# Performance work log

Hardware: AMD Instinct MI355X
Metric: run time of the kernel (lower is better)

## Reference

```python
import jax, jax.numpy as jnp
import numpy as np

B, Wd, C, H, F = 48, 88, 256, 32, 1024
NH_SELF, NH_CROSS = 8, 8


def _ln(x, g, b, eps=1e-5):
    mu = x.mean(-1, keepdims=True)
    var = ((x - mu) ** 2).mean(-1, keepdims=True)
    return (x - mu) / jnp.sqrt(var + eps) * g + b


def setup_inputs() -> dict:
    key = jax.random.key(0)
    ks = jax.random.split(key, 16)
    s = 0.02  # weight init scale
    d = {
        'pooled_features': jax.random.normal(ks[0], (B, Wd, C), jnp.float32),
        'features': jax.random.normal(ks[1], (B, C, H, Wd), jnp.float32),
        'self_pe': jax.random.normal(ks[2], (Wd, C), jnp.float32),
        'cross_pe': jax.random.normal(ks[3], (H, C), jnp.float32),
    }
    # LayerNorm params
    for n in ['ln_qs', 'ln_vs', 'ln_qc', 'ln_kv', 'ln_vc', 'ln_ffn']:
        d[n + '_g'] = jnp.ones((C,), jnp.float32)
        d[n + '_b'] = jnp.zeros((C,), jnp.float32)
    # attention projections (stored [in,out]; y = x @ W + b)
    names = ['Wq_s', 'Wk_s', 'Wv_s', 'Wp_s', 'Wq_c', 'Wk_c', 'Wv_c', 'Wp_c']
    for i, n in enumerate(names):
        d[n] = jax.random.normal(ks[4 + i], (C, C), jnp.float32) * s
    for n in ['bq_s', 'bv_s', 'bp_s', 'bq_c', 'bv_c', 'bp_c']:
        d[n] = jnp.zeros((C,), jnp.float32)
    # FFN
    d['W1'] = jax.random.normal(ks[12], (C, F), jnp.float32) * s
    d['b1'] = jnp.zeros((F,), jnp.float32)
    d['W2'] = jax.random.normal(ks[13], (F, C), jnp.float32) * s
    d['b2'] = jnp.zeros((C,), jnp.float32)
    return d


def reference(pooled_features, features, self_pe, cross_pe,
              ln_qs_g, ln_qs_b, ln_vs_g, ln_vs_b,
              ln_qc_g, ln_qc_b, ln_kv_g, ln_kv_b, ln_vc_g, ln_vc_b,
              ln_ffn_g, ln_ffn_b,
              Wq_s, bq_s, Wk_s, Wv_s, bv_s, Wp_s, bp_s,
              Wq_c, bq_c, Wk_c, Wv_c, bv_c, Wp_c, bp_c,
              W1, b1, W2, b2):
    b, w, c = pooled_features.shape
    h = features.shape[2]
    ds = c // NH_SELF
    dc = c // NH_CROSS

    # ---- cross attention first (op_order='cross_first', with_pe=True) ----
    xq = pooled_features                                  # [B,W,C]
    qn = _ln(xq, ln_qc_g, ln_qc_b)
    kv = jnp.transpose(features, (0, 3, 2, 1))            # [B,W,H,C]
    kn = _ln(kv + cross_pe[None, None], ln_kv_g, ln_kv_b)
    vn = _ln(kv, ln_vc_g, ln_vc_b)
    q = (qn @ Wq_c + bq_c).reshape(b, w, NH_CROSS, dc)    # query len 1 per column
    k = (kn @ Wk_c).reshape(b, w, h, NH_CROSS, dc)
    v = (vn @ Wv_c + bv_c).reshape(b, w, h, NH_CROSS, dc)
    attn = jnp.einsum('bwhd,bwkhd->bwhk', q, k) * (dc ** -0.5)
    attn = jax.nn.softmax(attn, axis=-1)
    out = jnp.einsum('bwhk,bwkhd->bwhd', attn, v).reshape(b, w, c)
    x = out @ Wp_c + bp_c + xq

    # ---- self attention over width tokens ----
    qn = _ln(x + self_pe[None], ln_qs_g, ln_qs_b)
    vn = _ln(x, ln_vs_g, ln_vs_b)
    q = (qn @ Wq_s + bq_s).reshape(b, w, NH_SELF, ds)
    k = (qn @ Wk_s).reshape(b, w, NH_SELF, ds)
    v = (vn @ Wv_s + bv_s).reshape(b, w, NH_SELF, ds)
    attn = jnp.einsum('bnhd,bmhd->bhnm', q, k) * (ds ** -0.5)
    attn = jax.nn.softmax(attn, axis=-1)
    out = jnp.einsum('bhnm,bmhd->bnhd', attn, v).reshape(b, w, c)
    x = out @ Wp_s + bp_s + x

    # ---- FFN (mmcv FFN, num_fcs=2, GELU, identity residual) ----
    hdn = _ln(x, ln_ffn_g, ln_ffn_b)
    hdn = jax.nn.gelu(hdn @ W1 + b1, approximate=False) @ W2 + b2
    return x + hdn
```

## Files before the change

kernel.cpp:

```cpp
#include <hip/hip_runtime.h>
#include <math.h>

#define B_   48
#define W_   88
#define C_   256
#define H_   32
#define F_   1024
#define BW_  (B_ * W_)
#define BWH_ (B_ * W_ * H_)
#define HW_  (H_ * W_)

typedef float  f32x4  __attribute__((ext_vector_type(4)));
typedef __bf16 bf16x8 __attribute__((ext_vector_type(8)));

__device__ __forceinline__ unsigned short f2bf(float f) {
  union { float f; unsigned int u; } v; v.f = f;
  unsigned int r = v.u + 0x7FFFu + ((v.u >> 16) & 1u);
  return (unsigned short)(r >> 16);
}
__device__ __forceinline__ float bf2f(unsigned short h) {
  union { unsigned int u; float f; } v; v.u = ((unsigned int)h) << 16;
  return v.f;
}
__device__ __forceinline__ unsigned int pack2(float a, float b) {
  return (unsigned int)f2bf(a) | ((unsigned int)f2bf(b) << 16);
}

__global__ __launch_bounds__(256) void prep_all(
    const float* __restrict__ Wq_s, const float* __restrict__ Wk_s,
    const float* __restrict__ Wv_s, const float* __restrict__ Wp_s,
    const float* __restrict__ W1, const float* __restrict__ W2,
    const float* __restrict__ Wq_c, const float* __restrict__ Wk_c,
    const float* __restrict__ Wv_c, const float* __restrict__ Wp_c,
    const float* __restrict__ bq_s, const float* __restrict__ bv_s,
    const float* __restrict__ bq_c, const float* __restrict__ bv_c,
    const float* __restrict__ bp_c,
    const float* __restrict__ pooled,
    const float* __restrict__ ln_qc_g, const float* __restrict__ ln_qc_b,
    const float* __restrict__ cross_pe,
    unsigned short* __restrict__ wqkvs, unsigned short* __restrict__ wps,
    unsigned short* __restrict__ w1t, unsigned short* __restrict__ w2t,
    unsigned short* __restrict__ mqk, unsigned short* __restrict__ mvp,
    float* __restrict__ bqk, float* __restrict__ bvp,
    float* __restrict__ bqkvs, unsigned short* __restrict__ qn_c,
    float* __restrict__ pes) {
  __shared__ float smem[256 * 33 + 4 * 33];
  int blk = blockIdx.x, t = threadIdx.x;

  if (blk < 768) {
    const float* src; unsigned short* dst; int Cc, R, tile;
    if (blk < 64)       { src = Wq_s; dst = wqkvs;          Cc = 256;  R = 256;  tile = blk; }
    else if (blk < 128) { src = Wk_s; dst = wqkvs + 65536;  Cc = 256;  R = 256;  tile = blk - 64; }
    else if (blk < 192) { src = Wv_s; dst = wqkvs + 131072; Cc = 256;  R = 256;  tile = blk - 128; }
    else if (blk < 256) { src = Wp_s; dst = wps;            Cc = 256;  R = 256;  tile = blk - 192; }
    else if (blk < 512) { src = W1;   dst = w1t;            Cc = 1024; R = 256;  tile = blk - 256; }
    else                { src = W2;   dst = w2t;            Cc = 256;  R = 1024; tile = blk - 512; }
    int tcn = Cc >> 5;
    int tr = tile / tcn, tc = tile % tcn;
    float (*lds)[33] = (float(*)[33])smem;
    int r = t >> 3, c4 = (t & 7) * 4;
    float4 v = *(const float4*)(src + (size_t)(tr * 32 + r) * Cc + tc * 32 + c4);
    lds[r][c4 + 0] = v.x; lds[r][c4 + 1] = v.y; lds[r][c4 + 2] = v.z; lds[r][c4 + 3] = v.w;
    __syncthreads();
    int rd = t >> 3, cd4 = (t & 7) * 4;
    unsigned int u0 = pack2(lds[cd4 + 0][rd], lds[cd4 + 1][rd]);
    unsigned int u1 = pack2(lds[cd4 + 2][rd], lds[cd4 + 3][rd]);
    uint2 u; u.x = u0; u.y = u1;
    *(uint2*)(dst + (size_t)(tc * 32 + rd) * R + tr * 32 + cd4) = u;
  } else if (blk < 1280) {
    int lb = blk - 768;
    int h = lb >> 6, cb = lb & 63;
    float (*wq)[33] = (float(*)[33])smem;
    float (*wk)[33] = (float(*)[33])(smem + 256 * 33);
#pragma unroll
    for (int p = 0; p < 8; p++) {
      int dp = (t >> 3) + 32 * p, d4 = (t & 7) * 4;
      float4 v = *(const float4*)(Wq_c + (size_t)dp * 256 + 32 * h + d4);
      wq[dp][d4 + 0] = v.x; wq[dp][d4 + 1] = v.y; wq[dp][d4 + 2] = v.z; wq[dp][d4 + 3] = v.w;
    }
    if (t < 128) {
      int c_l = t >> 5, dd = t & 31;
      wk[c_l][dd] = Wk_c[(size_t)(cb * 4 + c_l) * 256 + 32 * h + dd];
    }
    __syncthreads();
    const float scale = 0.17677669529663689f;
    int c_l = t >> 6, ln = t & 63;
    int n = 256 * h + cb * 4 + c_l;
#pragma unroll
    for (int j = 0; j < 4; j++) {
      int dp = ln + 64 * j;
      float acc = 0.f;
#pragma unroll
      for (int dd = 0; dd < 32; dd++) acc += wq[dp][dd] * wk[c_l][dd];
      mqk[(size_t)n * 256 + dp] = f2bf(acc * scale);
    }
    if (ln == 0) {
      float bb = 0.f;
#pragma unroll
      for (int dd = 0; dd < 32; dd++) bb += bq_c[32 * h + dd] * wk[c_l][dd];
      bqk[n] = bb * scale;
    }
  } else if (blk < 1792) {
    int lb = blk - 1280;
    int h = lb >> 6, db = lb & 63;
    float (*wv)[33] = (float(*)[33])smem;
    float (*wp)[33] = (float(*)[33])(smem + 256 * 33);
#pragma unroll
    for (int p = 0; p < 8; p++) {
      int c = (t >> 3) + 32 * p, d4 = (t & 7) * 4;
      float4 v = *(const float4*)(Wv_c + (size_t)c * 256 + 32 * h + d4);
      wv[c][d4 + 0] = v.x; wv[c][d4 + 1] = v.y; wv[c][d4 + 2] = v.z; wv[c][d4 + 3] = v.w;
    }
    if (t < 128) {
      int d_l = t >> 5, dd = t & 31;
      wp[d_l][dd] = Wp_c[(size_t)(32 * h + dd) * 256 + db * 4 + d_l];
    }
    __syncthreads();
    int d_l = t >> 6, ln = t & 63;
    int d = db * 4 + d_l;
#pragma unroll
    for (int j = 0; j < 4; j++) {
      int c = ln + 64 * j;
      float acc = 0.f;
#pragma unroll
      for (int dd = 0; dd < 32; dd++) acc += wv[c][dd] * wp[d_l][dd];
      mvp[(size_t)d * 2048 + 256 * h + c] = f2bf(acc);
    }
  } else if (blk == 1792) {
    float acc = bp_c[t];
    for (int dp = 0; dp < 256; dp++) acc += bv_c[dp] * Wp_c[(size_t)dp * 256 + t];
    bvp[t] = acc;
    bqkvs[t] = bq_s[t]; bqkvs[256 + t] = 0.f; bqkvs[512 + t] = bv_s[t];
  } else if (blk < 6017) {
    int row = blk - 1793, c = t;
    float v = pooled[(size_t)row * C_ + c];
    float s1 = v, s2 = v * v;
#pragma unroll
    for (int m = 32; m > 0; m >>= 1) {
      s1 += __shfl_xor(s1, m, 64); s2 += __shfl_xor(s2, m, 64);
    }
    float* red = smem;
    int wave = c >> 6;
    if ((c & 63) == 0) { red[wave] = s1; red[4 + wave] = s2; }
    __syncthreads();
    s1 = red[0] + red[1] + red[2] + red[3];
    s2 = red[4] + red[5] + red[6] + red[7];
    float mu = s1 * (1.f / C_);
    float rs = rsqrtf(s2 * (1.f / C_) - mu * mu + 1e-5f);
    qn_c[(size_t)row * C_ + c] = f2bf((v - mu) * rs * ln_qc_g[c] + ln_qc_b[c]);
  } else {
    int h = t >> 3, seg = t & 7;
    const float* pr = cross_pe + (size_t)h * 256 + seg * 32;
    float s1 = 0.f, s2 = 0.f;
#pragma unroll
    for (int i = 0; i < 32; i++) { float v = pr[i]; s1 += v; s2 += v * v; }
    s1 += __shfl_xor(s1, 1, 8); s2 += __shfl_xor(s2, 1, 8);
    s1 += __shfl_xor(s1, 2, 8); s2 += __shfl_xor(s2, 2, 8);
    s1 += __shfl_xor(s1, 4, 8); s2 += __shfl_xor(s2, 4, 8);
    if (seg == 0) { pes[2 * h] = s1; pes[2 * h + 1] = s2; }
  }
}

__global__ __launch_bounds__(128, 2) void cross_fused(
    const float* __restrict__ features, const float* __restrict__ cross_pe,
    const unsigned short* __restrict__ qt_g,
    const float* __restrict__ g_kv, const float* __restrict__ b_kv,
    const float* __restrict__ g_vc, const float* __restrict__ b_vc,
    const float* __restrict__ pes,
    unsigned short* __restrict__ ctx_g) {
  __shared__ __attribute__((aligned(16))) float stage[2 * 4 * 268];
  const int p = blockIdx.x;
  const int xcd = p & 7, slot = p >> 3;
  const int b = xcd + 8 * (slot / 22);
  const int w0 = (slot % 22) * 4;
  const int t = threadIdx.x;
  const int bw0 = b * 88 + w0;
  const int w = t >> 5, c8 = t & 31, cbase = c8 << 3;

  float qg[8][8], Qg[8], Qb[8];
  {
    float gk8[8], bk8[8];
    float4 u0 = *(const float4*)(g_kv + cbase), u1 = *(const float4*)(g_kv + cbase + 4);
    gk8[0]=u0.x; gk8[1]=u0.y; gk8[2]=u0.z; gk8[3]=u0.w;
    gk8[4]=u1.x; gk8[5]=u1.y; gk8[6]=u1.z; gk8[7]=u1.w;
    u0 = *(const float4*)(b_kv + cbase); u1 = *(const float4*)(b_kv + cbase + 4);
    bk8[0]=u0.x; bk8[1]=u0.y; bk8[2]=u0.z; bk8[3]=u0.w;
    bk8[4]=u1.x; bk8[5]=u1.y; bk8[6]=u1.z; bk8[7]=u1.w;
    const unsigned short* qrow = qt_g + (size_t)(bw0 + w) * 2048 + cbase;
#pragma unroll
    for (int hd = 0; hd < 8; hd++) {
      bf16x8 qv = *(const bf16x8*)(qrow + hd * 256);
      float sg = 0.f, sb = 0.f;
#pragma unroll
      for (int i = 0; i < 8; i++) {
        float qf = (float)qv[i];
        qg[hd][i] = qf * gk8[i];
        sg += qg[hd][i];
        sb += qf * bk8[i];
      }
      Qg[hd] = sg; Qb[hd] = sb;
    }
#pragma unroll
    for (int m = 1; m < 32; m <<= 1) {
#pragma unroll
      for (int hd = 0; hd < 8; hd++) {
        Qg[hd] += __shfl_xor(Qg[hd], m, 32);
        Qb[hd] += __shfl_xor(Qb[hd], m, 32);
      }
    }
  }

  float accA[8][8];
  float accB[8], l[8];
#pragma unroll
  for (int hd = 0; hd < 8; hd++) {
    accB[hd] = 0.f; l[hd] = 0.f;
#pragma unroll
    for (int i = 0; i < 8; i++) accA[hd][i] = 0.f;
  }

  const float* fbase = features + (size_t)b * (C_ * HW_) + w0;
  float4 x0 = *(const float4*)(fbase + (size_t)t * HW_);
  float4 x1 = *(const float4*)(fbase + (size_t)(t + 128) * HW_);
  float4 y0 = *(const float4*)(fbase + (size_t)t * HW_ + 88);
  float4 y1 = *(const float4*)(fbase + (size_t)(t + 128) * HW_ + 88);

#pragma unroll 2
  for (int h = 0; h < 32; ++h) {
    float* st = stage + (h & 1) * (4 * 268);
    st[0 * 268 + t] = x0.x; st[1 * 268 + t] = x0.y;
    st[2 * 268 + t] = x0.z; st[3 * 268 + t] = x0.w;
    st[0 * 268 + 128 + t] = x1.x; st[1 * 268 + 128 + t] = x1.y;
    st[2 * 268 + 128 + t] = x1.z; st[3 * 268 + 128 + t] = x1.w;
    asm volatile("s_waitcnt lgkmcnt(0)" ::: "memory");
    __builtin_amdgcn_s_barrier();
    asm volatile("" ::: "memory");
    if (h < 30) {
      x0 = *(const float4*)(fbase + (size_t)t * HW_ + (h + 2) * 88);
      x1 = *(const float4*)(fbase + (size_t)(t + 128) * HW_ + (h + 2) * 88);
    }
    const float* sr = st + w * 268 + cbase;
    float4 v0 = *(const float4*)(sr);
    float4 v1 = *(const float4*)(sr + 4);
    float vls[8] = {v0.x, v0.y, v0.z, v0.w, v1.x, v1.y, v1.z, v1.w};
    float4 q0 = *(const float4*)(cross_pe + h * 256 + cbase);
    float4 q1 = *(const float4*)(cross_pe + h * 256 + cbase + 4);
    float pe8[8] = {q0.x, q0.y, q0.z, q0.w, q1.x, q1.y, q1.z, q1.w};
    float s1 = 0.f, s2 = 0.f, sp = 0.f;
    float vp[8];
#pragma unroll
    for (int i = 0; i < 8; i++) {
      float v = vls[i];
      vp[i] = v + pe8[i];
      s1 += v; s2 += v * v; sp += v * pe8[i];
    }
    float S[8];
#pragma unroll
    for (int hd = 0; hd < 8; hd++) {
      float a = 0.f;
#pragma unroll
      for (int i = 0; i < 8; i++) a += qg[hd][i] * vp[i];
      S[hd] = a;
    }
#pragma unroll
    for (int m = 1; m < 32; m <<= 1) {
      s1 += __shfl_xor(s1, m, 32);
      s2 += __shfl_xor(s2, m, 32);
      sp += __shfl_xor(sp, m, 32);
#pragma unroll
      for (int hd = 0; hd < 8; hd++) S[hd] += __shfl_xor(S[hd], m, 32);
    }
    float mu_v = s1 * (1.f / 256.f);
    float rs_v = rsqrtf(s2 * (1.f / 256.f) - mu_v * mu_v + 1e-5f);
    float mu_k = (s1 + pes[2 * h]) * (1.f / 256.f);
    float rs_k = rsqrtf((s2 + 2.f * sp + pes[2 * h + 1]) * (1.f / 256.f)
                        - mu_k * mu_k + 1e-5f);
#pragma unroll
    for (int hd = 0; hd < 8; hd++) {
      float sc = rs_k * (S[hd] - mu_k * Qg[hd]) + Qb[hd];
      float e = __expf(sc);
      float er = e * rs_v;
      l[hd] += e;
      accB[hd] += er * mu_v;
#pragma unroll
      for (int i = 0; i < 8; i++) accA[hd][i] += er * vls[i];
    }
    float4 t0 = x0, t1 = x1;
    x0 = y0; x1 = y1;
    y0 = t0; y1 = t1;
  }
  float gv8[8], bv8[8];
  {
    float4 u0 = *(const float4*)(g_vc + cbase), u1 = *(const float4*)(g_vc + cbase + 4);
    gv8[0]=u0.x; gv8[1]=u0.y; gv8[2]=u0.z; gv8[3]=u0.w;
    gv8[4]=u1.x; gv8[5]=u1.y; gv8[6]=u1.z; gv8[7]=u1.w;
    u0 = *(const float4*)(b_vc + cbase); u1 = *(const float4*)(b_vc + cbase + 4);
    bv8[0]=u0.x; bv8[1]=u0.y; bv8[2]=u0.z; bv8[3]=u0.w;
    bv8[4]=u1.x; bv8[5]=u1.y; bv8[6]=u1.z; bv8[7]=u1.w;
  }
  unsigned short* orow = ctx_g + (size_t)(bw0 + w) * 2048 + cbase;
#pragma unroll
  for (int hd = 0; hd < 8; hd++) {
    float inv = 1.f / l[hd];
    unsigned short pk[8];
#pragma unroll
    for (int i = 0; i < 8; i++)
      pk[i] = f2bf(gv8[i] * (accA[hd][i] - accB[hd]) * inv + bv8[i]);
    *(uint4*)(orow + hd * 256) = *(uint4*)pk;
  }
}

__global__ __launch_bounds__(256) void ln_rows(
    const float* __restrict__ x,
    const float* __restrict__ g, const float* __restrict__ bta,
    unsigned short* __restrict__ out) {
  int row = blockIdx.x, c = threadIdx.x;
  float v = x[(size_t)row * C_ + c];
  float s1 = v, s2 = v * v;
#pragma unroll
  for (int m = 32; m > 0; m >>= 1) {
    s1 += __shfl_xor(s1, m, 64);
    s2 += __shfl_xor(s2, m, 64);
  }
  __shared__ float red[8];
  int wave = c >> 6;
  if ((c & 63) == 0) { red[wave] = s1; red[4 + wave] = s2; }
  __syncthreads();
  s1 = red[0] + red[1] + red[2] + red[3];
  s2 = red[4] + red[5] + red[6] + red[7];
  float mu = s1 * (1.f / C_);
  float rs = rsqrtf(s2 * (1.f / C_) - mu * mu + 1e-5f);
  out[(size_t)row * C_ + c] = f2bf((v - mu) * rs * g[c] + bta[c]);
}

__global__ __launch_bounds__(256) void ln_dual(
    const float* __restrict__ x, const float* __restrict__ pe,
    const float* __restrict__ g1, const float* __restrict__ b1a,
    const float* __restrict__ g2, const float* __restrict__ b2a,
    unsigned short* __restrict__ out1, unsigned short* __restrict__ out2) {
  int row = blockIdx.x, c = threadIdx.x;
  float v = x[(size_t)row * C_ + c];
  float vp = v + pe[(size_t)(row % 88) * C_ + c];
  float s1 = v, s2 = v * v, t1 = vp, t2 = vp * vp;
#pragma unroll
  for (int m = 32; m > 0; m >>= 1) {
    s1 += __shfl_xor(s1, m, 64); s2 += __shfl_xor(s2, m, 64);
    t1 += __shfl_xor(t1, m, 64); t2 += __shfl_xor(t2, m, 64);
  }
  __shared__ float red[16];
  int wave = c >> 6;
  if ((c & 63) == 0) {
    red[wave] = s1; red[4 + wave] = s2; red[8 + wave] = t1; red[12 + wave] = t2;
  }
  __syncthreads();
  s1 = red[0] + red[1] + red[2] + red[3];
  s2 = red[4] + red[5] + red[6] + red[7];
  t1 = red[8] + red[9] + red[10] + red[11];
  t2 = red[12] + red[13] + red[14] + red[15];
  float mu = s1 * (1.f / C_), rs = rsqrtf(s2 * (1.f / C_) - mu * mu + 1e-5f);
  float mup = t1 * (1.f / C_), rsp = rsqrtf(t2 * (1.f / C_) - mup * mup + 1e-5f);
  out1[(size_t)row * C_ + c] = f2bf((vp - mup) * rsp * g1[c] + b1a[c]);
  out2[(size_t)row * C_ + c] = f2bf((v - mu) * rs * g2[c] + b2a[c]);
}

__global__ __launch_bounds__(256) void gemm_bt(
    const unsigned short* __restrict__ A, const unsigned short* __restrict__ Bt,
    int M, int N, int K,
    const float* __restrict__ bias, const float* __restrict__ resid,
    float* __restrict__ outF, unsigned short* __restrict__ outB, int act_gelu) {
  __shared__ __attribute__((aligned(16))) unsigned short As[64][32];
  __shared__ __attribute__((aligned(16))) unsigned short Bs[64][32];
  const int tiles_n = N >> 6;
  const int bm = blockIdx.x / tiles_n;
  const int bn = blockIdx.x % tiles_n;
  const int tid = threadIdx.x;
  const int wave = tid >> 6, lane = tid & 63;
  const int quad = lane >> 4, lr = lane & 15;
  const int wm = (wave >> 1) << 5, wn = (wave & 1) << 5;
  const int lrow = tid >> 2;
  const int lcol = (tid & 3) << 3;
  const size_t a_base = (size_t)(bm * 64 + lrow) * K + lcol;
  const size_t b_base = (size_t)(bn * 64 + lrow) * K + lcol;
  f32x4 acc[2][2] = {};
  uint4 areg = *(const uint4*)(A + a_base);
  uint4 breg = *(const uint4*)(Bt + b_base);
  for (int k0 = 0; k0 < K; k0 += 32) {
    *(uint4*)&As[lrow][lcol] = areg;
    *(uint4*)&Bs[lrow][lcol] = breg;
    __syncthreads();
    if (k0 + 32 < K) {
      areg = *(const uint4*)(A + a_base + k0 + 32);
      breg = *(const uint4*)(Bt + b_base + k0 + 32);
    }
    bf16x8 af0 = *(const bf16x8*)&As[wm + lr][quad << 3];
    bf16x8 af1 = *(const bf16x8*)&As[wm + 16 + lr][quad << 3];
    bf16x8 bf0 = *(const bf16x8*)&Bs[wn + lr][quad << 3];
    bf16x8 bf1 = *(const bf16x8*)&Bs[wn + 16 + lr][quad << 3];
    acc[0][0] = __builtin_amdgcn_mfma_f32_16x16x32_bf16(af0, bf0, acc[0][0], 0, 0, 0);
    acc[0][1] = __builtin_amdgcn_mfma_f32_16x16x32_bf16(af0, bf1, acc[0][1], 0, 0, 0);
    acc[1][0] = __builtin_amdgcn_mfma_f32_16x16x32_bf16(af1, bf0, acc[1][0], 0, 0, 0);
    acc[1][1] = __builtin_amdgcn_mfma_f32_16x16x32_bf16(af1, bf1, acc[1][1], 0, 0, 0);
    __syncthreads();
  }
#pragma unroll
  for (int i = 0; i < 2; i++)
#pragma unroll
    for (int j = 0; j < 2; j++)
#pragma unroll
      for (int rr = 0; rr < 4; rr++) {
        int row = bm * 64 + wm + i * 16 + quad * 4 + rr;
        int col = bn * 64 + wn + j * 16 + lr;
        float val = acc[i][j][rr];
        if (bias) val += bias[col];
        if (act_gelu) val = 0.5f * val * (1.f + erff(val * 0.70710678118654752f));
        if (resid) val += resid[(size_t)row * N + col];
        if (outF) outF[(size_t)row * N + col] = val;
        else outB[(size_t)row * N + col] = f2bf(val);
      }
}

__global__ __launch_bounds__(256) void gemm_bt_st(
    const unsigned short* __restrict__ A, const unsigned short* __restrict__ Bt,
    int M, int N, int K, int ldc,
    const float* __restrict__ bias, float* __restrict__ outF) {
  __shared__ __attribute__((aligned(16))) unsigned short As[64][32];
  __shared__ __attribute__((aligned(16))) unsigned short Bs[64][32];
  const int tiles_n = N >> 6;
  const int bm = blockIdx.x / tiles_n;
  const int bn = blockIdx.x % tiles_n;
  const int tid = threadIdx.x;
  const int wave = tid >> 6, lane = tid & 63;
  const int quad = lane >> 4, lr = lane & 15;
  const int wm = (wave >> 1) << 5, wn = (wave & 1) << 5;
  const int lrow = tid >> 2;
  const int lcol = (tid & 3) << 3;
  const size_t a_base = (size_t)(bm * 64 + lrow) * K + lcol;
  const size_t b_base = (size_t)(bn * 64 + lrow) * K + lcol;
  f32x4 acc[2][2] = {};
  uint4 areg = *(const uint4*)(A + a_base);
  uint4 breg = *(const uint4*)(Bt + b_base);
  for (int k0 = 0; k0 < K; k0 += 32) {
    *(uint4*)&As[lrow][lcol] = areg;
    *(uint4*)&Bs[lrow][lcol] = breg;
    __syncthreads();
    if (k0 + 32 < K) {
      areg = *(const uint4*)(A + a_base + k0 + 32);
      breg = *(const uint4*)(Bt + b_base + k0 + 32);
    }
    bf16x8 af0 = *(const bf16x8*)&As[wm + lr][quad << 3];
    bf16x8 af1 = *(const bf16x8*)&As[wm + 16 + lr][quad << 3];
    bf16x8 bf0 = *(const bf16x8*)&Bs[wn + lr][quad << 3];
    bf16x8 bf1 = *(const bf16x8*)&Bs[wn + 16 + lr][quad << 3];
    acc[0][0] = __builtin_amdgcn_mfma_f32_16x16x32_bf16(af0, bf0, acc[0][0], 0, 0, 0);
    acc[0][1] = __builtin_amdgcn_mfma_f32_16x16x32_bf16(af0, bf1, acc[0][1], 0, 0, 0);
    acc[1][0] = __builtin_amdgcn_mfma_f32_16x16x32_bf16(af1, bf0, acc[1][0], 0, 0, 0);
    acc[1][1] = __builtin_amdgcn_mfma_f32_16x16x32_bf16(af1, bf1, acc[1][1], 0, 0, 0);
    __syncthreads();
  }
#pragma unroll
  for (int i = 0; i < 2; i++)
#pragma unroll
    for (int j = 0; j < 2; j++)
#pragma unroll
      for (int rr = 0; rr < 4; rr++) {
        int row = bm * 64 + wm + i * 16 + quad * 4 + rr;
        int col = bn * 64 + wn + j * 16 + lr;
        outF[(size_t)row * ldc + col] = acc[i][j][rr] + bias[col];
      }
}

__global__ __launch_bounds__(192) void self_attn3(
    const float* __restrict__ qkv, unsigned short* __restrict__ out) {
  int b = blockIdx.x >> 3;
  int h = blockIdx.x & 7;
  int t = threadIdx.x;
  __shared__ float kl[88][33];
  __shared__ float vl[88][33];
  for (int i = t; i < 704; i += 192) {
    int m = i >> 3, d4 = (i & 7) << 2;
    float4 kv4 = *(const float4*)(qkv + (size_t)(b * 88 + m) * 768 + 256 + h * 32 + d4);
    float4 vv4 = *(const float4*)(qkv + (size_t)(b * 88 + m) * 768 + 512 + h * 32 + d4);
    kl[m][d4 + 0] = kv4.x; kl[m][d4 + 1] = kv4.y; kl[m][d4 + 2] = kv4.z; kl[m][d4 + 3] = kv4.w;
    vl[m][d4 + 0] = vv4.x; vl[m][d4 + 1] = vv4.y; vl[m][d4 + 2] = vv4.z; vl[m][d4 + 3] = vv4.w;
  }
  __syncthreads();
  int r = t >> 1, dh = t & 1;
  if (r < 88) {
    const float* qrow = qkv + (size_t)(b * 88 + r) * 768 + h * 32;
    float qr[32];
#pragma unroll
    for (int g = 0; g < 8; g++) {
      float4 q4 = *(const float4*)(qrow + g * 4);
      qr[g * 4 + 0] = q4.x; qr[g * 4 + 1] = q4.y; qr[g * 4 + 2] = q4.z; qr[g * 4 + 3] = q4.w;
    }
    float sreg[44];
    float mx = -1e30f;
    int m0 = dh * 44;
    for (int mi = 0; mi < 44; mi++) {
      const float* krow = kl[m0 + mi];
      float s = 0.f;
#pragma unroll
      for (int d = 0; d < 32; d++) s += qr[d] * krow[d];
      s *= 0.17677669529663689f;
      sreg[mi] = s;
      mx = fmaxf(mx, s);
    }
    mx = fmaxf(mx, __shfl_xor(mx, 1, 64));
    float sum = 0.f;
    for (int mi = 0; mi < 44; mi++) { float e = __expf(sreg[mi] - mx); sreg[mi] = e; sum += e; }
    sum += __shfl_xor(sum, 1, 64);
    float inv = 1.f / sum;
    float o[32];
#pragma unroll
    for (int d = 0; d < 32; d++) o[d] = 0.f;
    for (int mi = 0; mi < 44; mi++) {
      float p = sreg[mi] * inv;
      const float* vrow = vl[m0 + mi];
#pragma unroll
      for (int d = 0; d < 32; d++) o[d] += p * vrow[d];
    }
#pragma unroll
    for (int d = 0; d < 32; d++) o[d] += __shfl_xor(o[d], 1, 64);
    unsigned short* orow = out + (size_t)(b * 88 + r) * 256 + h * 32 + dh * 16;
    uint4 u0, u1;
    int d0 = dh * 16;
    u0.x = pack2(o[d0 + 0], o[d0 + 1]);  u0.y = pack2(o[d0 + 2], o[d0 + 3]);
    u0.z = pack2(o[d0 + 4], o[d0 + 5]);  u0.w = pack2(o[d0 + 6], o[d0 + 7]);
    u1.x = pack2(o[d0 + 8], o[d0 + 9]);  u1.y = pack2(o[d0 + 10], o[d0 + 11]);
    u1.z = pack2(o[d0 + 12], o[d0 + 13]); u1.w = pack2(o[d0 + 14], o[d0 + 15]);
    *(uint4*)(orow) = u0;
    *(uint4*)(orow + 8) = u1;
  }
}

extern "C" void kernel_launch(void* const* d_in, const int* in_sizes, int n_in,
                              void* d_out, int out_size, void* d_ws, size_t ws_size,
                              hipStream_t stream) {
  (void)in_sizes; (void)n_in; (void)out_size; (void)ws_size;
  const float* pooled   = (const float*)d_in[0];
  const float* features = (const float*)d_in[1];
  const float* self_pe  = (const float*)d_in[2];
  const float* cross_pe = (const float*)d_in[3];
  const float* ln_qs_g = (const float*)d_in[4],  *ln_qs_b = (const float*)d_in[5];
  const float* ln_vs_g = (const float*)d_in[6],  *ln_vs_b = (const float*)d_in[7];
  const float* ln_qc_g = (const float*)d_in[8],  *ln_qc_b = (const float*)d_in[9];
  const float* ln_kv_g = (const float*)d_in[10], *ln_kv_b = (const float*)d_in[11];
  const float* ln_vc_g = (const float*)d_in[12], *ln_vc_b = (const float*)d_in[13];
  const float* ln_ffn_g = (const float*)d_in[14], *ln_ffn_b = (const float*)d_in[15];
  const float* Wq_s = (const float*)d_in[16], *Wk_s = (const float*)d_in[17];
  const float* Wv_s = (const float*)d_in[18], *Wp_s = (const float*)d_in[19];
  const float* Wq_c = (const float*)d_in[20], *Wk_c = (const float*)d_in[21];
  const float* Wv_c = (const float*)d_in[22], *Wp_c = (const float*)d_in[23];
  const float* bq_s = (const float*)d_in[24], *bv_s = (const float*)d_in[25];
  const float* bp_s = (const float*)d_in[26], *bq_c = (const float*)d_in[27];
  const float* bv_c = (const float*)d_in[28], *bp_c = (const float*)d_in[29];
  const float* W1 = (const float*)d_in[30], *b1 = (const float*)d_in[31];
  const float* W2 = (const float*)d_in[32], *b2 = (const float*)d_in[33];
  float* outp = (float*)d_out;
  char* ws = (char*)d_ws;

  size_t off = 0;
  auto alloc = [&](size_t bytes) { size_t o = off; off = (off + bytes + 255) & ~(size_t)255; return o; };
  size_t QT  = alloc((size_t)BW_ * 2048 * 2);
  size_t CTX = alloc((size_t)BW_ * 2048 * 2);
  size_t MQK = alloc((size_t)2048 * 256 * 2);
  size_t MVP = alloc((size_t)256 * 2048 * 2);
  size_t BQK = alloc(2048 * 4);
  size_t BVP = alloc(256 * 4);
  size_t WQKVS = alloc((size_t)768 * 256 * 2);
  size_t BQKVS = alloc(768 * 4);
  size_t WPS = alloc(65536 * 2);
  size_t W1T = alloc(262144 * 2), W2T = alloc(262144 * 2);
  size_t QN_C = alloc((size_t)BW_ * C_ * 2);
  size_t PES  = alloc(64 * 4);
  size_t X1    = alloc((size_t)BW_ * C_ * 4);
  size_t QN_S  = alloc((size_t)BW_ * C_ * 2);
  size_t VN_S  = alloc((size_t)BW_ * C_ * 2);
  size_t QKV_S = alloc((size_t)BW_ * 768 * 4);
  size_t S_O   = alloc((size_t)BW_ * C_ * 2);
  size_t X2    = alloc((size_t)BW_ * C_ * 4);
  size_t FFN   = alloc((size_t)BW_ * C_ * 2);
  size_t H1    = alloc((size_t)BW_ * F_ * 2);

  unsigned short* qt   = (unsigned short*)(ws + QT);
  unsigned short* ctx  = (unsigned short*)(ws + CTX);
  unsigned short* mqk  = (unsigned short*)(ws + MQK);
  unsigned short* mvp  = (unsigned short*)(ws + MVP);
  float* bqk = (float*)(ws + BQK);
  float* bvp = (float*)(ws + BVP);
  unsigned short* wqkvs = (unsigned short*)(ws + WQKVS);
  float* bqkvs = (float*)(ws + BQKVS);
  unsigned short* wps = (unsigned short*)(ws + WPS);
  unsigned short* w1t = (unsigned short*)(ws + W1T), *w2t = (unsigned short*)(ws + W2T);
  unsigned short* qn_c = (unsigned short*)(ws + QN_C);
  float* pes = (float*)(ws + PES);
  float*          x1   = (float*)(ws + X1);
  unsigned short* qn_s = (unsigned short*)(ws + QN_S);
  unsigned short* vn_s = (unsigned short*)(ws + VN_S);
  float* qkv_s = (float*)(ws + QKV_S);
  unsigned short* s_o  = (unsigned short*)(ws + S_O);
  float*          x2   = (float*)(ws + X2);
  unsigned short* ffn_n = (unsigned short*)(ws + FFN);
  unsigned short* h1    = (unsigned short*)(ws + H1);

  prep_all<<<6018, 256, 0, stream>>>(
      Wq_s, Wk_s, Wv_s, Wp_s, W1, W2, Wq_c, Wk_c, Wv_c, Wp_c,
      bq_s, bv_s, bq_c, bv_c, bp_c, pooled, ln_qc_g, ln_qc_b, cross_pe,
      wqkvs, wps, w1t, w2t, mqk, mvp, bqk, bvp, bqkvs, qn_c, pes);

  gemm_bt<<<(BW_ / 64) * (2048 / 64), 256, 0, stream>>>(qn_c, mqk, BW_, 2048, 256,
      bqk, nullptr, nullptr, qt, 0);

  cross_fused<<<1056, 128, 0, stream>>>(features, cross_pe, qt,
      ln_kv_g, ln_kv_b, ln_vc_g, ln_vc_b, pes, ctx);

  gemm_bt<<<(BW_ / 64) * (C_ / 64), 256, 0, stream>>>(ctx, mvp, BW_, C_, 2048,
      bvp, pooled, x1, nullptr, 0);

  ln_dual<<<BW_, 256, 0, stream>>>(x1, self_pe, ln_qs_g, ln_qs_b,
                                   ln_vs_g, ln_vs_b, qn_s, vn_s);

  gemm_bt_st<<<(BW_ / 64) * (512 / 64), 256, 0, stream>>>(qn_s, wqkvs, BW_, 512, 256,
      768, bqkvs, qkv_s);
  gemm_bt_st<<<(BW_ / 64) * (256 / 64), 256, 0, stream>>>(vn_s, wqkvs + 131072, BW_, 256, 256,
      768, bqkvs + 512, qkv_s + 512);

  self_attn3<<<B_ * 8, 192, 0, stream>>>(qkv_s, s_o);

  gemm_bt<<<(BW_ / 64) * (C_ / 64), 256, 0, stream>>>(s_o, wps, BW_, C_, C_,
      bp_s, x1, x2, nullptr, 0);

  ln_rows<<<BW_, 256, 0, stream>>>(x2, ln_ffn_g, ln_ffn_b, ffn_n);
  gemm_bt<<<(BW_ / 64) * (F_ / 64), 256, 0, stream>>>(ffn_n, w1t, BW_, F_, C_,
      b1, nullptr, nullptr, h1, 1);
  gemm_bt<<<(BW_ / 64) * (C_ / 64), 256, 0, stream>>>(h1, w2t, BW_, C_, F_,
      b2, x2, outp, nullptr, 0);
}
```

Baseline: 504.4 us.

## Software-pipeline cross-attention loop: overlap shuffle reductions with next row compute

Restructures the per-h loop of the cross-attention kernel into a software pipeline. The cross-lane shuffle reductions and softmax/accumulate for row h-1 are interleaved with the LDS read and partial dot products for row h, and the cross_pe row is prefetched one step ahead. This hides shuffle and LDS latency behind independent arithmetic. The cost is more live registers (previous partials, vprev, peC/peN), which could lower occupancy, and the loop unroll pragma is removed.

```diff
diff --git a/kernel.cpp b/kernel.cpp
--- a/kernel.cpp
+++ b/kernel.cpp
@@ -225,8 +225,63 @@
   float4 y0 = *(const float4*)(fbase + (size_t)t * HW_ + 88);
   float4 y1 = *(const float4*)(fbase + (size_t)(t + 128) * HW_ + 88);
 
-#pragma unroll 2
-  for (int h = 0; h < 32; ++h) {
+  float peC[8];
+  {
+    float4 q0 = *(const float4*)(cross_pe + cbase);
+    float4 q1 = *(const float4*)(cross_pe + cbase + 4);
+    peC[0]=q0.x; peC[1]=q0.y; peC[2]=q0.z; peC[3]=q0.w;
+    peC[4]=q1.x; peC[5]=q1.y; peC[6]=q1.z; peC[7]=q1.w;
+  }
+  float pesC1 = pes[0], pesC2 = pes[1];
+
+  float ps1, ps2, pu, pS[8], vprev[8];
+
+  {
+    float* st = stage;
+    st[0 * 268 + t] = x0.x; st[1 * 268 + t] = x0.y;
+    st[2 * 268 + t] = x0.z; st[3 * 268 + t] = x0.w;
+    st[0 * 268 + 128 + t] = x1.x; st[1 * 268 + 128 + t] = x1.y;
+    st[2 * 268 + 128 + t] = x1.z; st[3 * 268 + 128 + t] = x1.w;
+    asm volatile("s_waitcnt lgkmcnt(0)" ::: "memory");
+    __builtin_amdgcn_s_barrier();
+    asm volatile("" ::: "memory");
+    x0 = *(const float4*)(fbase + (size_t)t * HW_ + 2 * 88);
+    x1 = *(const float4*)(fbase + (size_t)(t + 128) * HW_ + 2 * 88);
+    const float* sr = st + w * 268 + cbase;
+    float4 v0 = *(const float4*)(sr);
+    float4 v1 = *(const float4*)(sr + 4);
+    float vls[8] = {v0.x, v0.y, v0.z, v0.w, v1.x, v1.y, v1.z, v1.w};
+    float peN[8];
+    {
+      float4 q0 = *(const float4*)(cross_pe + 256 + cbase);
+      float4 q1 = *(const float4*)(cross_pe + 256 + cbase + 4);
+      peN[0]=q0.x; peN[1]=q0.y; peN[2]=q0.z; peN[3]=q0.w;
+      peN[4]=q1.x; peN[5]=q1.y; peN[6]=q1.z; peN[7]=q1.w;
+    }
+    float s1 = 0.f, s2 = 0.f, sp = 0.f, vp[8];
+#pragma unroll
+    for (int i = 0; i < 8; i++) {
+      float v = vls[i];
+      vp[i] = v + peC[i];
+      s1 += v; s2 += v * v; sp += v * peC[i];
+    }
+#pragma unroll
+    for (int hd = 0; hd < 8; hd++) {
+      float a = 0.f;
+#pragma unroll
+      for (int i = 0; i < 8; i++) a += qg[hd][i] * vp[i];
+      pS[hd] = a;
+    }
+    ps1 = s1; ps2 = s2; pu = s2 + 2.f * sp;
+#pragma unroll
+    for (int i = 0; i < 8; i++) vprev[i] = vls[i];
+    float4 t0 = x0, t1 = x1;
+    x0 = y0; x1 = y1; y0 = t0; y1 = t1;
+#pragma unroll
+    for (int i = 0; i < 8; i++) peC[i] = peN[i];
+  }
+
+  for (int h = 1; h < 32; ++h) {
     float* st = stage + (h & 1) * (4 * 268);
     st[0 * 268 + t] = x0.x; st[1 * 268 + t] = x0.y;
     st[2 * 268 + t] = x0.z; st[3 * 268 + t] = x0.w;
@@ -242,53 +297,91 @@
     const float* sr = st + w * 268 + cbase;
     float4 v0 = *(const float4*)(sr);
     float4 v1 = *(const float4*)(sr + 4);
+#pragma unroll
+    for (int m = 1; m < 32; m <<= 1) {
+      ps1 += __shfl_xor(ps1, m, 32);
+      ps2 += __shfl_xor(ps2, m, 32);
+      pu  += __shfl_xor(pu, m, 32);
+#pragma unroll
+      for (int hd = 0; hd < 8; hd++) pS[hd] += __shfl_xor(pS[hd], m, 32);
+    }
+    float peN[8];
+    if (h < 31) {
+      float4 q0 = *(const float4*)(cross_pe + (h + 1) * 256 + cbase);
+      float4 q1 = *(const float4*)(cross_pe + (h + 1) * 256 + cbase + 4);
+      peN[0]=q0.x; peN[1]=q0.y; peN[2]=q0.z; peN[3]=q0.w;
+      peN[4]=q1.x; peN[5]=q1.y; peN[6]=q1.z; peN[7]=q1.w;
+    } else {
+#pragma unroll
+      for (int i = 0; i < 8; i++) peN[i] = 0.f;
+    }
     float vls[8] = {v0.x, v0.y, v0.z, v0.w, v1.x, v1.y, v1.z, v1.w};
-    float4 q0 = *(const float4*)(cross_pe + h * 256 + cbase);
-    float4 q1 = *(const float4*)(cross_pe + h * 256 + cbase + 4);
-    float pe8[8] = {q0.x, q0.y, q0.z, q0.w, q1.x, q1.y, q1.z, q1.w};
-    float s1 = 0.f, s2 = 0.f, sp = 0.f;
-    float vp[8];
+    float s1 = 0.f, s2 = 0.f, sp = 0.f, vp[8];
 #pragma unroll
     for (int i = 0; i < 8; i++) {
       float v = vls[i];
-      vp[i] = v + pe8[i];
-      s1 += v; s2 += v * v; sp += v * pe8[i];
-    }
-    float S[8];
+      vp[i] = v + peC[i];
+      s1 += v; s2 += v * v; sp += v * peC[i];
+    }
+    float nS[8];
 #pragma unroll
     for (int hd = 0; hd < 8; hd++) {
       float a = 0.f;
 #pragma unroll
       for (int i = 0; i < 8; i++) a += qg[hd][i] * vp[i];
-      S[hd] = a;
-    }
+      nS[hd] = a;
+    }
+    {
+      float mu_v = ps1 * (1.f / 256.f);
+      float rs_v = rsqrtf(ps2 * (1.f / 256.f) - mu_v * mu_v + 1e-5f);
+      float mu_k = (ps1 + pesC1) * (1.f / 256.f);
+      float rs_k = rsqrtf((pu + pesC2) * (1.f / 256.f) - mu_k * mu_k + 1e-5f);
+#pragma unroll
+      for (int hd = 0; hd < 8; hd++) {
+        float sc = rs_k * (pS[hd] - mu_k * Qg[hd]) + Qb[hd];
+        float e = __expf(sc);
+        float er = e * rs_v;
+        l[hd] += e;
+        accB[hd] += er * mu_v;
+#pragma unroll
+        for (int i = 0; i < 8; i++) accA[hd][i] += er * vprev[i];
+      }
+    }
+    ps1 = s1; ps2 = s2; pu = s2 + 2.f * sp;
+#pragma unroll
+    for (int hd = 0; hd < 8; hd++) pS[hd] = nS[hd];
+#pragma unroll
+    for (int i = 0; i < 8; i++) { vprev[i] = vls[i]; peC[i] = peN[i]; }
+    pesC1 = pes[2 * h]; pesC2 = pes[2 * h + 1];
+    float4 t0 = x0, t1 = x1;
+    x0 = y0; x1 = y1; y0 = t0; y1 = t1;
+  }
+
+  {
 #pragma unroll
     for (int m = 1; m < 32; m <<= 1) {
-      s1 += __shfl_xor(s1, m, 32);
-      s2 += __shfl_xor(s2, m, 32);
-      sp += __shfl_xor(sp, m, 32);
-#pragma unroll
-      for (int hd = 0; hd < 8; hd++) S[hd] += __shfl_xor(S[hd], m, 32);
-    }
-    float mu_v = s1 * (1.f / 256.f);
-    float rs_v = rsqrtf(s2 * (1.f / 256.f) - mu_v * mu_v + 1e-5f);
-    float mu_k = (s1 + pes[2 * h]) * (1.f / 256.f);
-    float rs_k = rsqrtf((s2 + 2.f * sp + pes[2 * h + 1]) * (1.f / 256.f)
-                        - mu_k * mu_k + 1e-5f);
+      ps1 += __shfl_xor(ps1, m, 32);
+      ps2 += __shfl_xor(ps2, m, 32);
+      pu  += __shfl_xor(pu, m, 32);
+#pragma unroll
+      for (int hd = 0; hd < 8; hd++) pS[hd] += __shfl_xor(pS[hd], m, 32);
+    }
+    float mu_v = ps1 * (1.f / 256.f);
+    float rs_v = rsqrtf(ps2 * (1.f / 256.f) - mu_v * mu_v + 1e-5f);
+    float mu_k = (ps1 + pesC1) * (1.f / 256.f);
+    float rs_k = rsqrtf((pu + pesC2) * (1.f / 256.f) - mu_k * mu_k + 1e-5f);
 #pragma unroll
     for (int hd = 0; hd < 8; hd++) {
-      float sc = rs_k * (S[hd] - mu_k * Qg[hd]) + Qb[hd];
+      float sc = rs_k * (pS[hd] - mu_k * Qg[hd]) + Qb[hd];
       float e = __expf(sc);
       float er = e * rs_v;
       l[hd] += e;
       accB[hd] += er * mu_v;
 #pragma unroll
-      for (int i = 0; i < 8; i++) accA[hd][i] += er * vls[i];
-    }
-    float4 t0 = x0, t1 = x1;
-    x0 = y0; x1 = y1;
-    y0 = t0; y1 = t1;
-  }
+      for (int i = 0; i < 8; i++) accA[hd][i] += er * vprev[i];
+    }
+  }
+
   float gv8[8], bv8[8];
   {
     float4 u0 = *(const float4*)(g_vc + cbase), u1 = *(const float4*)(g_vc + cbase + 4);
```

New measurement: 500.4 us. No clear change (-0.8%).
